# Kernel tuning notes

Hardware: AMD Instinct MI355X
Metric: run time of the kernel (lower is better)

Reference implementation:

```python
import jax, jax.numpy as jnp
import numpy as np

B, S, D, H = 4, 2048, 1024, 16
HD = D // H

def setup_inputs() -> dict:
    key = jax.random.key(0)
    ks = jax.random.split(key, 5)
    s = 1.0 / np.sqrt(D)
    return {
        "x": jax.random.normal(ks[0], (B, S, D), dtype=jnp.float32),
        "Wq": jax.random.normal(ks[1], (D, D), dtype=jnp.float32) * s,
        "Wk": jax.random.normal(ks[2], (D, D), dtype=jnp.float32) * s,
        "Wv": jax.random.normal(ks[3], (D, D), dtype=jnp.float32) * s,
        "Wo": jax.random.normal(ks[4], (D, D), dtype=jnp.float32) * s,
        "bo": jnp.zeros((D,), dtype=jnp.float32),
    }

def reference(x, Wq, Wk, Wv, Wo, bo):
    b, n, _ = x.shape
    # torch Linear: x @ W.T ; split heads -> [b, h, n, hd]
    def proj(W):
        return (x @ W.T).reshape(b, n, H, HD).transpose(0, 2, 1, 3)
    q, k, v = proj(Wq), proj(Wk), proj(Wv)
    scores = jnp.einsum('bhqd,bhkd->bhqk', q, k)  # [b,h,n,n]
    causal = jnp.triu(jnp.ones((n, n), dtype=bool), k=1)
    scores = jnp.where(causal, -jnp.inf, scores)
    attn = jax.nn.softmax(scores / np.sqrt(HD), axis=-1)  # dropout p=0.0 (eval)
    ctx = jnp.einsum('bhqk,bhkd->bhqd', attn, v)
    ctx = ctx.transpose(0, 2, 1, 3).reshape(b, n, D)
    return ctx @ Wo.T + bo
```

## Files before the change

kernel.cpp:

```cpp
#include <hip/hip_runtime.h>
#include <stdint.h>
#include <cmath>

#define BATCH 4
#define SEQ   2048
#define DM    1024
#define NH    16
#define HDIM  64
#define MROWS (BATCH*SEQ)
#define NQB   16

typedef __attribute__((ext_vector_type(8)))  __bf16 bf16x8;
typedef __attribute__((ext_vector_type(8)))  unsigned short u16x8;
typedef __attribute__((ext_vector_type(4)))  float f32x4;
typedef __attribute__((ext_vector_type(16))) float f32x16;
typedef __attribute__((ext_vector_type(4)))  unsigned int u32x4;

__device__ __forceinline__ unsigned short f2bf(float f) {
  unsigned u = __float_as_uint(f);
  u = (u + 0x7FFFu + ((u >> 16) & 1u)) >> 16;
  return (unsigned short)u;
}

__device__ __forceinline__ f32x4 mfma_bf16(bf16x8 a, bf16x8 b, f32x4 c) {
  return __builtin_amdgcn_mfma_f32_16x16x32_bf16(a, b, c, 0, 0, 0);
}
__device__ __forceinline__ f32x16 mfma32(bf16x8 a, bf16x8 b, f32x16 c) {
  return __builtin_amdgcn_mfma_f32_32x32x16_bf16(a, b, c, 0, 0, 0);
}

__device__ __forceinline__ unsigned cvtpk(float lo, float hi) {
  unsigned r;
  asm("v_cvt_pk_bf16_f32 %0, %1, %2" : "=v"(r) : "v"(lo), "v"(hi));
  return r;
}
__device__ __forceinline__ void permswap(unsigned &a, unsigned &b) {
  asm volatile("v_permlane32_swap_b32 %0, %1" : "+v"(a), "+v"(b));
}
__device__ __forceinline__ float exp2v(float x) {
  float r;
  asm("v_exp_f32 %0, %1" : "=v"(r) : "v"(x));
  return r;
}
__device__ __forceinline__ f32x16 zero16() {
  f32x16 z;
#pragma unroll
  for (int i = 0; i < 16; ++i) z[i] = 0.f;
  return z;
}

typedef const __attribute__((address_space(1))) unsigned int* as1_u32p;
typedef __attribute__((address_space(3))) unsigned int* as3_u32p;

__device__ __forceinline__ void gload16(const void* g, void* l) {
  __builtin_amdgcn_global_load_lds((as1_u32p)g, (as3_u32p)l, 16, 0, 0);
}

__global__ void cvt_f32_bf16(const float* __restrict__ src,
                             unsigned short* __restrict__ dst, int n4) {
  int i = blockIdx.x * blockDim.x + threadIdx.x;
  int stride = gridDim.x * blockDim.x;
  for (; i < n4; i += stride) {
    float4 v = ((const float4*)src)[i];
    ushort4 o;
    o.x = f2bf(v.x); o.y = f2bf(v.y); o.z = f2bf(v.z); o.w = f2bf(v.w);
    ((ushort4*)dst)[i] = o;
  }
}

__global__ void cvt_w4(const float* __restrict__ s0, const float* __restrict__ s1,
                       const float* __restrict__ s2, const float* __restrict__ s3,
                       unsigned short* __restrict__ d0, unsigned short* __restrict__ d1,
                       unsigned short* __restrict__ d2, unsigned short* __restrict__ d3,
                       int n4) {
  const float* src = (blockIdx.y == 0) ? s0 : (blockIdx.y == 1) ? s1 : (blockIdx.y == 2) ? s2 : s3;
  unsigned short* dst = (blockIdx.y == 0) ? d0 : (blockIdx.y == 1) ? d1 : (blockIdx.y == 2) ? d2 : d3;
  int i = blockIdx.x * blockDim.x + threadIdx.x;
  int stride = gridDim.x * blockDim.x;
  for (; i < n4; i += stride) {
    float4 v = ((const float4*)src)[i];
    ushort4 o;
    o.x = f2bf(v.x); o.y = f2bf(v.y); o.z = f2bf(v.z); o.w = f2bf(v.w);
    ((ushort4*)dst)[i] = o;
  }
}

__device__ __forceinline__ void gemm_tile_mainloop(
    const unsigned short* __restrict__ A, const unsigned short* __restrict__ Bw,
    int rowBase, int colBase,
    unsigned short* As, unsigned short* Bs,
    f32x4 acc[4][4], int tid)
{
  const int wid = tid >> 6, lane = tid & 63;
  const int wm = wid >> 1, wn = wid & 1;

  const unsigned short* aSrc[4];
  const unsigned short* bSrc[4];
  int ldsDst[4];
#pragma unroll
  for (int j = 0; j < 4; ++j) {
    int c = j * 256 + tid;
    int row = c >> 3;
    int inB = (c & 7) * 16;
    int off = row * DM + ((inB ^ ((row & 7) << 4)) >> 1);
    aSrc[j] = A + (size_t)rowBase * DM + off;
    bSrc[j] = Bw + (size_t)colBase * DM + off;
    ldsDst[j] = (j * 256 + wid * 64) * 8;
  }

  auto stage = [&](int buf) {
#pragma unroll
    for (int j = 0; j < 4; ++j) {
      gload16(aSrc[j], As + buf * 8192 + ldsDst[j]);
      aSrc[j] += 64;
    }
#pragma unroll
    for (int j = 0; j < 4; ++j) {
      gload16(bSrc[j], Bs + buf * 8192 + ldsDst[j]);
      bSrc[j] += 64;
    }
  };

  stage(0);
  asm volatile("s_waitcnt vmcnt(0)" ::: "memory");
  __builtin_amdgcn_s_barrier();

  for (int k0 = 0; k0 < DM; k0 += 64) {
    const int cur = (k0 >> 6) & 1;
    if (k0 + 64 < DM) stage(cur ^ 1);

    const char* Ab = (const char*)As + cur * 16384;
    const char* Bb = (const char*)Bs + cur * 16384;
#pragma unroll
    for (int s2 = 0; s2 < 2; ++s2) {
      bf16x8 af[4], bfv[4];
#pragma unroll
      for (int m = 0; m < 4; ++m) {
        int row = wm * 64 + m * 16 + (lane & 15);
        int off = row * 128 + ((s2 * 64 + ((lane >> 4) * 16)) ^ ((row & 7) << 4));
        af[m] = *(const bf16x8*)(Ab + off);
      }
#pragma unroll
      for (int n = 0; n < 4; ++n) {
        int row = wn * 64 + n * 16 + (lane & 15);
        int off = row * 128 + ((s2 * 64 + ((lane >> 4) * 16)) ^ ((row & 7) << 4));
        bfv[n] = *(const bf16x8*)(Bb + off);
      }
#pragma unroll
      for (int m = 0; m < 4; ++m)
#pragma unroll
        for (int n = 0; n < 4; ++n)
          acc[m][n] = mfma_bf16(af[m], bfv[n], acc[m][n]);
    }
    asm volatile("s_waitcnt vmcnt(0)" ::: "memory");
    __builtin_amdgcn_s_barrier();
  }
}

__global__ __launch_bounds__(256, 2) void gemm_qkv(
    const unsigned short* __restrict__ xb,
    const unsigned short* __restrict__ Wqb, const unsigned short* __restrict__ Wkb,
    const unsigned short* __restrict__ Wvb,
    unsigned short* __restrict__ Qd, unsigned short* __restrict__ Kd,
    unsigned short* __restrict__ Vd)
{
  __shared__ unsigned short As[2 * 128 * 64];
  __shared__ unsigned short Bs[2 * 128 * 64];
  const int tid = threadIdx.x;
  const int z = blockIdx.z;
  const unsigned short* W = (z == 0) ? Wqb : (z == 1) ? Wkb : Wvb;
  unsigned short* dst = (z == 0) ? Qd : (z == 1) ? Kd : Vd;
  const int rowBase = blockIdx.x * 128, colBase = blockIdx.y * 128;

  f32x4 acc[4][4];
#pragma unroll
  for (int m = 0; m < 4; ++m)
#pragma unroll
    for (int n = 0; n < 4; ++n) acc[m][n] = (f32x4){0.f, 0.f, 0.f, 0.f};

  gemm_tile_mainloop(xb, W, rowBase, colBase, As, Bs, acc, tid);

  const int wid = tid >> 6, lane = tid & 63;
  const int wm = wid >> 1, wn = wid & 1;
#pragma unroll
  for (int m = 0; m < 4; ++m)
#pragma unroll
    for (int n = 0; n < 4; ++n)
#pragma unroll
      for (int r = 0; r < 4; ++r) {
        int grow = rowBase + wm * 64 + m * 16 + ((lane >> 4) * 4) + r;
        int gcol = colBase + wn * 64 + n * 16 + (lane & 15);
        int b = grow >> 11, s = grow & (SEQ - 1);
        int h = gcol >> 6, hd = gcol & 63;
        dst[(((size_t)(b * NH + h)) * SEQ + s) * HDIM + hd] = f2bf(acc[m][n][r]);
      }
}

__global__ __launch_bounds__(256, 2) void gemm_out(
    const unsigned short* __restrict__ ctx, const unsigned short* __restrict__ Wob,
    const float* __restrict__ bo, float* __restrict__ out)
{
  __shared__ unsigned short As[2 * 128 * 64];
  __shared__ unsigned short Bs[2 * 128 * 64];
  const int tid = threadIdx.x;
  const int rowBase = blockIdx.x * 128, colBase = blockIdx.y * 128;

  f32x4 acc[4][4];
#pragma unroll
  for (int m = 0; m < 4; ++m)
#pragma unroll
    for (int n = 0; n < 4; ++n) acc[m][n] = (f32x4){0.f, 0.f, 0.f, 0.f};

  gemm_tile_mainloop(ctx, Wob, rowBase, colBase, As, Bs, acc, tid);

  const int wid = tid >> 6, lane = tid & 63;
  const int wm = wid >> 1, wn = wid & 1;
#pragma unroll
  for (int m = 0; m < 4; ++m)
#pragma unroll
    for (int n = 0; n < 4; ++n)
#pragma unroll
      for (int r = 0; r < 4; ++r) {
        int grow = rowBase + wm * 64 + m * 16 + ((lane >> 4) * 4) + r;
        int gcol = colBase + wn * 64 + n * 16 + (lane & 15);
        out[(size_t)grow * DM + gcol] = acc[m][n][r] + bo[gcol];
      }
}

__global__ void transpose_v(const unsigned short* __restrict__ Vd,
                            unsigned short* __restrict__ VT)
{
  __shared__ unsigned short tile[64 * 72];
  const int tid = threadIdx.x;
  const int bh = blockIdx.y, s0 = blockIdx.x * 64;
  const unsigned short* src = Vd + (size_t)bh * SEQ * HDIM + (size_t)s0 * HDIM;
#pragma unroll
  for (int j = 0; j < 2; ++j) {
    int c = j * 256 + tid;
    int r = c >> 3, c0 = (c & 7) * 8;
    *(u16x8*)(tile + r * 72 + c0) = *(const u16x8*)(src + r * HDIM + c0);
  }
  __syncthreads();
  unsigned short* dst = VT + (size_t)bh * HDIM * SEQ + s0;
#pragma unroll
  for (int j = 0; j < 2; ++j) {
    int c = j * 256 + tid;
    int d = c >> 3, c0 = (c & 7) * 8;
    u16x8 v;
#pragma unroll
    for (int e = 0; e < 8; ++e) v[e] = tile[(c0 + e) * 72 + d];
    *(u16x8*)(dst + (size_t)d * SEQ + c0) = v;
  }
}

__global__ __launch_bounds__(256, 2) void attn_fwd3(
    const unsigned short* __restrict__ Qg, const unsigned short* __restrict__ Kg,
    const unsigned short* __restrict__ VTg, unsigned short* __restrict__ ctx)
{
  __shared__ unsigned short smem[24576];

  const int tid = threadIdx.x, wid = tid >> 6, lane = tid & 63;
  const int hi = lane >> 5, lq = lane & 31;
  const int bh = blockIdx.y;
  const unsigned short* Qp = Qg  + (size_t)bh * SEQ * HDIM;
  const unsigned short* Kp = Kg  + (size_t)bh * SEQ * HDIM;
  const unsigned short* Vp = VTg + (size_t)bh * HDIM * SEQ;
  const int b = bh >> 4, h = bh & 15;
  const float C2 = 0.18033688f;

  int sRow[2], sSwz[2], sDst[2];
#pragma unroll
  for (int j = 0; j < 2; ++j) {
    int c = j * 256 + tid;
    sRow[j] = c >> 3;
    sSwz[j] = (((c & 7) * 16) ^ ((sRow[j] & 7) << 4)) >> 1;
    sDst[j] = (j * 256 + wid * 64) * 8;
  }
  int off0[4], off1[4];
#pragma unroll
  for (int ks = 0; ks < 4; ++ks) {
    int col = ks * 32 + hi * 16;
    off0[ks] = lq * 128 + (col ^ ((lq & 7) << 4));
    off1[ks] = (lq + 32) * 128 + (col ^ ((lq & 7) << 4));
  }

  for (int half = 0; half < 2; ++half) {
    const int qb = half == 0 ? (int)blockIdx.x : (NQB - 1 - (int)blockIdx.x);
    const int qw0 = qb * 128 + wid * 32;

    const unsigned short* kSrc[2];
    const unsigned short* vSrc[2];
#pragma unroll
    for (int j = 0; j < 2; ++j) {
      kSrc[j] = Kp + (size_t)sRow[j] * HDIM + sSwz[j];
      vSrc[j] = Vp + (size_t)sRow[j] * SEQ + sSwz[j];
    }
    auto stageKV = [&](int buf) {
#pragma unroll
      for (int j = 0; j < 2; ++j) {
        gload16(kSrc[j], smem + buf * 4096 + sDst[j]);
        kSrc[j] += 64 * HDIM;
      }
#pragma unroll
      for (int j = 0; j < 2; ++j) {
        gload16(vSrc[j], smem + 12288 + buf * 4096 + sDst[j]);
        vSrc[j] += 64;
      }
    };

    bf16x8 qf[4];
    {
      const unsigned short* qrow = Qp + (size_t)(qw0 + lq) * HDIM + hi * 8;
#pragma unroll
      for (int ks = 0; ks < 4; ++ks) qf[ks] = *(const bf16x8*)(qrow + ks * 16);
    }

    f32x16 o0 = zero16(), o1 = zero16();
    float m_run = -INFINITY, l_run = 0.f, mc2 = 0.f;
    const int nt = 2 * qb + 2;

    stageKV(0); stageKV(1);
    asm volatile("s_waitcnt vmcnt(4)" ::: "memory");
    __builtin_amdgcn_s_barrier();

    for (int t = 0; t < nt; ++t) {
      const int cur = t % 3;
      const bool pf = (t + 2) < nt;
      if (pf) stageKV((t + 2) % 3);

      if (t * 64 <= qw0 + 31) {
        const char* Kl = (const char*)smem + cur * 8192;
        f32x16 s0 = zero16(), s1 = zero16();
        __builtin_amdgcn_s_setprio(1);
#pragma unroll
        for (int ks = 0; ks < 4; ++ks) {
          bf16x8 a0 = *(const bf16x8*)(Kl + off0[ks]);
          bf16x8 a1 = *(const bf16x8*)(Kl + off1[ks]);
          s0 = mfma32(a0, qf[ks], s0);
          s1 = mfma32(a1, qf[ks], s1);
        }
        __builtin_amdgcn_s_setprio(0);

        if (t * 64 + 63 > qw0) {
          const int q = qw0 + lq;
          const int kb = t * 64 + 4 * hi;
#pragma unroll
          for (int r = 0; r < 16; ++r) {
            int k0 = kb + (r & 3) + 8 * (r >> 2);
            if (k0 > q)      s0[r] = -INFINITY;
            if (k0 + 32 > q) s1[r] = -INFINITY;
          }
        }

        float pmax = fmaxf(s0[0], s0[1]);
#pragma unroll
        for (int r = 2; r < 16; r += 2) pmax = fmaxf(pmax, fmaxf(s0[r], s0[r + 1]));
#pragma unroll
        for (int r = 0; r < 16; r += 2) pmax = fmaxf(pmax, fmaxf(s1[r], s1[r + 1]));
        pmax = fmaxf(pmax, __shfl_xor(pmax, 32, 64));

        if (!__all(pmax - m_run <= 64.0f)) {
          float mn = fmaxf(m_run, pmax);
          float alpha = exp2v((m_run - mn) * C2);
          l_run *= alpha;
#pragma unroll
          for (int r = 0; r < 16; ++r) { o0[r] *= alpha; o1[r] *= alpha; }
          m_run = mn;
          mc2 = mn * C2;
        }

        float rsum = 0.f;
#pragma unroll
        for (int r = 0; r < 16; ++r) {
          float p = exp2v(__builtin_fmaf(s0[r], C2, -mc2));
          s0[r] = p; rsum += p;
        }
#pragma unroll
        for (int r = 0; r < 16; ++r) {
          float p = exp2v(__builtin_fmaf(s1[r], C2, -mc2));
          s1[r] = p; rsum += p;
        }
        rsum += __shfl_xor(rsum, 32, 64);
        l_run += rsum;

        bf16x8 pfr[4];
#pragma unroll
        for (int h2 = 0; h2 < 2; ++h2) {
          {
            unsigned va = cvtpk(s0[h2 * 8 + 0], s0[h2 * 8 + 1]);
            unsigned vb = cvtpk(s0[h2 * 8 + 4], s0[h2 * 8 + 5]);
            unsigned vc = cvtpk(s0[h2 * 8 + 2], s0[h2 * 8 + 3]);
            unsigned vd = cvtpk(s0[h2 * 8 + 6], s0[h2 * 8 + 7]);
            permswap(va, vb); permswap(vc, vd);
            u32x4 tt; tt.x = va; tt.y = vc; tt.z = vb; tt.w = vd;
            pfr[h2] = __builtin_bit_cast(bf16x8, tt);
          }
          {
            unsigned va = cvtpk(s1[h2 * 8 + 0], s1[h2 * 8 + 1]);
            unsigned vb = cvtpk(s1[h2 * 8 + 4], s1[h2 * 8 + 5]);
            unsigned vc = cvtpk(s1[h2 * 8 + 2], s1[h2 * 8 + 3]);
            unsigned vd = cvtpk(s1[h2 * 8 + 6], s1[h2 * 8 + 7]);
            permswap(va, vb); permswap(vc, vd);
            u32x4 tt; tt.x = va; tt.y = vc; tt.z = vb; tt.w = vd;
            pfr[2 + h2] = __builtin_bit_cast(bf16x8, tt);
          }
        }

        const char* Vl = (const char*)smem + 24576 + cur * 8192;
        __builtin_amdgcn_s_setprio(1);
#pragma unroll
        for (int ks = 0; ks < 4; ++ks) {
          bf16x8 va0 = *(const bf16x8*)(Vl + off0[ks]);
          bf16x8 va1 = *(const bf16x8*)(Vl + off1[ks]);
          o0 = mfma32(va0, pfr[ks], o0);
          o1 = mfma32(va1, pfr[ks], o1);
        }
        __builtin_amdgcn_s_setprio(0);
      }

      if (pf) asm volatile("s_waitcnt vmcnt(4)" ::: "memory");
      else    asm volatile("s_waitcnt vmcnt(0)" ::: "memory");
      __builtin_amdgcn_s_barrier();
    }

    const float invl = 1.0f / l_run;
    unsigned short* Ot = smem;
    const int q = wid * 32 + lq;
#pragma unroll
    for (int r2 = 0; r2 < 16; r2 += 2) {
      int d = (r2 & 3) + 8 * (r2 >> 2) + 4 * hi;
      unsigned w0 = cvtpk(o0[r2] * invl, o0[r2 + 1] * invl);
      *(unsigned*)((char*)Ot + q * 128 + ((2 * d) ^ ((q & 7) << 4))) = w0;
      int d2 = d + 32;
      unsigned w1 = cvtpk(o1[r2] * invl, o1[r2 + 1] * invl);
      *(unsigned*)((char*)Ot + q * 128 + ((2 * d2) ^ ((q & 7) << 4))) = w1;
    }
    __syncthreads();

#pragma unroll
    for (int i = 0; i < 4; ++i) {
      int idx = i * 256 + tid;
      int qq = idx >> 3, c16 = (idx & 7) * 8;
      bf16x8 v = *(const bf16x8*)((const char*)Ot + qq * 128 + ((2 * c16) ^ ((qq & 7) << 4)));
      *(bf16x8*)(ctx + ((size_t)(b * SEQ) + qb * 128 + qq) * DM + h * 64 + c16) = v;
    }
    __syncthreads();
  }
}

extern "C" void kernel_launch(void* const* d_in, const int* in_sizes, int n_in,
                              void* d_out, int out_size, void* d_ws, size_t ws_size,
                              hipStream_t stream)
{
  (void)in_sizes; (void)n_in; (void)out_size; (void)ws_size;
  const float* x  = (const float*)d_in[0];
  const float* Wq = (const float*)d_in[1];
  const float* Wk = (const float*)d_in[2];
  const float* Wv = (const float*)d_in[3];
  const float* Wo = (const float*)d_in[4];
  const float* bo = (const float*)d_in[5];
  float* out = (float*)d_out;

  char* ws = (char*)d_ws;
  unsigned short* xb  = (unsigned short*)(ws);
  unsigned short* Wqb = (unsigned short*)(ws + (size_t)16 * 1048576);
  unsigned short* Wkb = (unsigned short*)(ws + (size_t)18 * 1048576);
  unsigned short* Wvb = (unsigned short*)(ws + (size_t)20 * 1048576);
  unsigned short* Wob = (unsigned short*)(ws + (size_t)22 * 1048576);
  unsigned short* Qd  = (unsigned short*)(ws + (size_t)24 * 1048576);
  unsigned short* Kd  = (unsigned short*)(ws + (size_t)40 * 1048576);
  unsigned short* Vd  = (unsigned short*)(ws + (size_t)56 * 1048576);
  unsigned short* ctxb= (unsigned short*)(ws + (size_t)72 * 1048576);
  unsigned short* VT  = xb;

  cvt_f32_bf16<<<2048, 256, 0, stream>>>(x, xb, MROWS * DM / 4);
  cvt_w4<<<dim3(64, 4), 256, 0, stream>>>(Wq, Wk, Wv, Wo, Wqb, Wkb, Wvb, Wob, DM * DM / 4);

  gemm_qkv<<<dim3(MROWS / 128, DM / 128, 3), 256, 0, stream>>>(xb, Wqb, Wkb, Wvb, Qd, Kd, Vd);
  transpose_v<<<dim3(SEQ / 64, BATCH * NH), 256, 0, stream>>>(Vd, VT);
  attn_fwd3<<<dim3(NQB / 2, BATCH * NH), 256, 0, stream>>>(Qd, Kd, VT, ctxb);
  gemm_out<<<dim3(MROWS / 128, DM / 128, 1), 256, 0, stream>>>(ctxb, Wob, bo, out);
}
```

Before: 253.6 us.

## Drop GEMM LDS double buffering and raise attention kernel occupancy bound

The shared GEMM main loop for the QKV and output projections moves from a two-stage double-buffered LDS pipeline to a single buffer. Each k-step now loads a tile, synchronizes, computes, and synchronizes again. This halves the LDS footprint per block, which could let more blocks fit per CU, but global loads no longer overlap with MFMA work. Separately, the attention kernel's launch bound goes from 2 to 3 blocks per CU. That tightens the register budget and risks spills.

```diff
diff --git a/kernel.cpp b/kernel.cpp
--- a/kernel.cpp
+++ b/kernel.cpp
@@ -93,44 +93,28 @@
 {
   const int wid = tid >> 6, lane = tid & 63;
   const int wm = wid >> 1, wn = wid & 1;
-
-  const unsigned short* aSrc[4];
-  const unsigned short* bSrc[4];
-  int ldsDst[4];
-#pragma unroll
-  for (int j = 0; j < 4; ++j) {
-    int c = j * 256 + tid;
-    int row = c >> 3;
-    int inB = (c & 7) * 16;
-    int off = row * DM + ((inB ^ ((row & 7) << 4)) >> 1);
-    aSrc[j] = A + (size_t)rowBase * DM + off;
-    bSrc[j] = Bw + (size_t)colBase * DM + off;
-    ldsDst[j] = (j * 256 + wid * 64) * 8;
-  }
-
-  auto stage = [&](int buf) {
+  const unsigned short* Atile = A + (size_t)rowBase * DM;
+  const unsigned short* Btile = Bw + (size_t)colBase * DM;
+
+  for (int k0 = 0; k0 < DM; k0 += 64) {
 #pragma unroll
     for (int j = 0; j < 4; ++j) {
-      gload16(aSrc[j], As + buf * 8192 + ldsDst[j]);
-      aSrc[j] += 64;
+      int c = j * 256 + tid;
+      int row = c >> 3;
+      int inB = (c & 7) * 16;
+      int srcE = row * DM + k0 + ((inB ^ ((row & 7) << 4)) >> 1);
+      gload16(Atile + srcE, As + (size_t)(j * 256 + wid * 64) * 8);
     }
 #pragma unroll
     for (int j = 0; j < 4; ++j) {
-      gload16(bSrc[j], Bs + buf * 8192 + ldsDst[j]);
-      bSrc[j] += 64;
-    }
-  };
-
-  stage(0);
-  asm volatile("s_waitcnt vmcnt(0)" ::: "memory");
-  __builtin_amdgcn_s_barrier();
-
-  for (int k0 = 0; k0 < DM; k0 += 64) {
-    const int cur = (k0 >> 6) & 1;
-    if (k0 + 64 < DM) stage(cur ^ 1);
-
-    const char* Ab = (const char*)As + cur * 16384;
-    const char* Bb = (const char*)Bs + cur * 16384;
+      int c = j * 256 + tid;
+      int row = c >> 3;
+      int inB = (c & 7) * 16;
+      int srcE = row * DM + k0 + ((inB ^ ((row & 7) << 4)) >> 1);
+      gload16(Btile + srcE, Bs + (size_t)(j * 256 + wid * 64) * 8);
+    }
+    __syncthreads();
+
 #pragma unroll
     for (int s2 = 0; s2 < 2; ++s2) {
       bf16x8 af[4], bfv[4];
@@ -138,13 +122,13 @@
       for (int m = 0; m < 4; ++m) {
         int row = wm * 64 + m * 16 + (lane & 15);
         int off = row * 128 + ((s2 * 64 + ((lane >> 4) * 16)) ^ ((row & 7) << 4));
-        af[m] = *(const bf16x8*)(Ab + off);
+        af[m] = *(const bf16x8*)((const char*)As + off);
       }
 #pragma unroll
       for (int n = 0; n < 4; ++n) {
         int row = wn * 64 + n * 16 + (lane & 15);
         int off = row * 128 + ((s2 * 64 + ((lane >> 4) * 16)) ^ ((row & 7) << 4));
-        bfv[n] = *(const bf16x8*)(Bb + off);
+        bfv[n] = *(const bf16x8*)((const char*)Bs + off);
       }
 #pragma unroll
       for (int m = 0; m < 4; ++m)
@@ -152,8 +136,7 @@
         for (int n = 0; n < 4; ++n)
           acc[m][n] = mfma_bf16(af[m], bfv[n], acc[m][n]);
     }
-    asm volatile("s_waitcnt vmcnt(0)" ::: "memory");
-    __builtin_amdgcn_s_barrier();
+    __syncthreads();
   }
 }
 
@@ -164,8 +147,8 @@
     unsigned short* __restrict__ Qd, unsigned short* __restrict__ Kd,
     unsigned short* __restrict__ Vd)
 {
-  __shared__ unsigned short As[2 * 128 * 64];
-  __shared__ unsigned short Bs[2 * 128 * 64];
+  __shared__ unsigned short As[128 * 64];
+  __shared__ unsigned short Bs[128 * 64];
   const int tid = threadIdx.x;
   const int z = blockIdx.z;
   const unsigned short* W = (z == 0) ? Wqb : (z == 1) ? Wkb : Wvb;
@@ -200,8 +183,8 @@
     const unsigned short* __restrict__ ctx, const unsigned short* __restrict__ Wob,
     const float* __restrict__ bo, float* __restrict__ out)
 {
-  __shared__ unsigned short As[2 * 128 * 64];
-  __shared__ unsigned short Bs[2 * 128 * 64];
+  __shared__ unsigned short As[128 * 64];
+  __shared__ unsigned short Bs[128 * 64];
   const int tid = threadIdx.x;
   const int rowBase = blockIdx.x * 128, colBase = blockIdx.y * 128;
 
@@ -253,7 +236,7 @@
   }
 }
 
-__global__ __launch_bounds__(256, 2) void attn_fwd3(
+__global__ __launch_bounds__(256, 3) void attn_fwd3(
     const unsigned short* __restrict__ Qg, const unsigned short* __restrict__ Kg,
     const unsigned short* __restrict__ VTg, unsigned short* __restrict__ ctx)
 {
```

Result: no change. 250.3 us (-1.3%).
